# Performance work log

Measured on AMD Instinct MI355X. Metric: run time of the kernel, lower is better.

The kernel has to match this reference:

```python
import jax, jax.numpy as jnp
import numpy as np
from functools import partial

T0, T1, N = 0.0, 1.0, 1024
B = 131072
R, SIGMA = 0.1, 0.2


def setup_inputs() -> dict:
    key = jax.random.key(0)
    k0, k1 = jax.random.split(key)
    Z0 = jax.random.uniform(k0, (B,), dtype=jnp.float32) + 49.5  # around Z0=50 in source
    W = jax.random.normal(k1, (B, N + 1), dtype=jnp.float32)     # Brownian increments (W[:,0] unused)
    Wf = jnp.full((1, 1), R, dtype=jnp.float32)                  # drift weight (f = Linear 1x1)
    Wg = jnp.full((1, 1), SIGMA, dtype=jnp.float32)              # diffusion weight (g = Linear 1x1)
    return {"Z0": Z0, "W": W, "Wf": Wf, "Wg": Wg}


def reference(Z0, W, Wf, Wg):
    # Z[i+1] = Z[i] + f(Z[i])*dt + g(Z[i])*sqrt(dt)*W[i+1], f(z)=Wf*z, g(z)=Wg*z
    dt = jnp.float32((T1 - T0) / N)
    sdt = jnp.sqrt(dt)
    r = Wf[0, 0]
    s = Wg[0, 0]

    def step(z, w):  # z: [B], w: [B]
        zn = z + r * z * dt + s * z * sdt * w
        return zn, zn

    # scan over the N time steps; noise transposed to [N, B]
    _, Zs = jax.lax.scan(step, Z0, jnp.swapaxes(W[:, 1:], 0, 1))
    Z = jnp.concatenate([Z0[:, None], jnp.swapaxes(Zs, 0, 1)], axis=1)  # [B, N+1]
    return Z, W
```

## Files before the change

kernel.cpp:

```cpp
#include <hip/hip_runtime.h>


__global__ __launch_bounds__(256) void em_prefix_kernel(
    const float* __restrict__ Z0,
    const float* __restrict__ W,
    const float* __restrict__ Wf,
    const float* __restrict__ Wg,
    float* __restrict__ Zout,
    float* __restrict__ Wout)
{
    constexpr int NP1  = 1025;
    constexpr int SEG  = 256;
    constexpr int NSEG = 4;

    const int b    = blockIdx.x;
    const int t    = threadIdx.x;
    const int lane = t & 63;
    const int wid  = t >> 6;

    const float dt  = 1.0f / 1024.0f;
    const float sdt = 0.03125f;
    const float a   = Wf[0] * dt;
    const float c   = Wg[0] * sdt;
    const float m0  = 1.0f + a;

    const size_t base = (size_t)b * (size_t)NP1;
    const float* __restrict__ wrow  = W    + base;
    float*       __restrict__ zrow  = Zout + base;
    float*       __restrict__ worow = Wout + base;

    float w[NSEG], m[NSEG];
    #pragma unroll
    for (int s = 0; s < NSEG; ++s) {
        w[s] = wrow[1 + s * SEG + t];
        m[s] = fmaf(c, w[s], m0);
    }

    __shared__ float wtot[NSEG][4];
    float p[NSEG];
    #pragma unroll
    for (int s = 0; s < NSEG; ++s) {
        float v = m[s];
        #pragma unroll
        for (int d = 1; d < 64; d <<= 1) {
            float o = __shfl_up(v, d, 64);
            if (lane >= d) v *= o;
        }
        p[s] = v;
        if (lane == 63) wtot[s][wid] = v;
    }
    __syncthreads();

    const float z0 = Z0[b];
    if (t == 0) {
        zrow[0]  = z0;
        worow[0] = wrow[0];
    }

    float C = z0;
    #pragma unroll
    for (int s = 0; s < NSEG; ++s) {
        float wpre = 1.0f;
        #pragma unroll
        for (int wv = 0; wv < 3; ++wv) {
            float tv = wtot[s][wv];
            if (wv < wid) wpre *= tv;
        }
        const int idx = 1 + s * SEG + t;
        zrow[idx]  = C * wpre * p[s];
        worow[idx] = w[s];
        C *= wtot[s][0] * wtot[s][1] * wtot[s][2] * wtot[s][3];
    }
}

extern "C" void kernel_launch(void* const* d_in, const int* in_sizes, int n_in,
                              void* d_out, int out_size, void* d_ws, size_t ws_size,
                              hipStream_t stream) {
    const float* Z0 = (const float*)d_in[0];
    const float* W  = (const float*)d_in[1];
    const float* Wf = (const float*)d_in[2];
    const float* Wg = (const float*)d_in[3];

    const int B   = in_sizes[0];
    const int NP1 = in_sizes[1] / B;

    float* Zout = (float*)d_out;
    float* Wout = Zout + (size_t)B * (size_t)NP1;

    em_prefix_kernel<<<B, 256, 0, stream>>>(Z0, W, Wf, Wg, Zout, Wout);
}
```

Measured before the change: 301.3 us.

## Use persistent blocks over multiple rows with prefetch and nontemporal memory ops

Switches from one block per row to 4096 blocks, each processing a contiguous range of rows. The loads for the next row's noise are issued before the current row's scan, so memory latency overlaps with compute. Double-buffered shared totals avoid a second barrier per row. All global loads and stores become nontemporal to reduce cache pollution in this streaming kernel. This trades parallelism and occupancy-based latency hiding for fewer block launches and explicit prefetch.

```diff
diff --git a/kernel.cpp b/kernel.cpp
--- a/kernel.cpp
+++ b/kernel.cpp
@@ -7,13 +7,13 @@
     const float* __restrict__ Wf,
     const float* __restrict__ Wg,
     float* __restrict__ Zout,
-    float* __restrict__ Wout)
+    float* __restrict__ Wout,
+    int B, int rowsPerBlock)
 {
     constexpr int NP1  = 1025;
     constexpr int SEG  = 256;
     constexpr int NSEG = 4;
 
-    const int b    = blockIdx.x;
     const int t    = threadIdx.x;
     const int lane = t & 63;
     const int wid  = t >> 6;
@@ -24,52 +24,73 @@
     const float c   = Wg[0] * sdt;
     const float m0  = 1.0f + a;
 
-    const size_t base = (size_t)b * (size_t)NP1;
-    const float* __restrict__ wrow  = W    + base;
-    float*       __restrict__ zrow  = Zout + base;
-    float*       __restrict__ worow = Wout + base;
+    __shared__ float wtot[2][NSEG][4];
 
-    float w[NSEG], m[NSEG];
-    #pragma unroll
-    for (int s = 0; s < NSEG; ++s) {
-        w[s] = wrow[1 + s * SEG + t];
-        m[s] = fmaf(c, w[s], m0);
+    const int r0 = blockIdx.x * rowsPerBlock;
+    const int r1 = min(r0 + rowsPerBlock, B);
+    if (r0 >= r1) return;
+
+    float wcur[NSEG];
+    {
+        const float* __restrict__ wrow = W + (size_t)r0 * NP1;
+        #pragma unroll
+        for (int s = 0; s < NSEG; ++s)
+            wcur[s] = __builtin_nontemporal_load(wrow + 1 + s * SEG + t);
     }
 
-    __shared__ float wtot[NSEG][4];
-    float p[NSEG];
-    #pragma unroll
-    for (int s = 0; s < NSEG; ++s) {
-        float v = m[s];
+    int parity = 0;
+    for (int r = r0; r < r1; ++r) {
+        float wnxt[NSEG];
+        const bool havenext = (r + 1 < r1);
+        if (havenext) {
+            const float* __restrict__ wrown = W + (size_t)(r + 1) * NP1;
+            #pragma unroll
+            for (int s = 0; s < NSEG; ++s)
+                wnxt[s] = __builtin_nontemporal_load(wrown + 1 + s * SEG + t);
+        }
+
+        float p[NSEG];
         #pragma unroll
-        for (int d = 1; d < 64; d <<= 1) {
-            float o = __shfl_up(v, d, 64);
-            if (lane >= d) v *= o;
+        for (int s = 0; s < NSEG; ++s) {
+            float v = fmaf(c, wcur[s], m0);
+            #pragma unroll
+            for (int d = 1; d < 64; d <<= 1) {
+                float o = __shfl_up(v, d, 64);
+                if (lane >= d) v *= o;
+            }
+            p[s] = v;
+            if (lane == 63) wtot[parity][s][wid] = v;
         }
-        p[s] = v;
-        if (lane == 63) wtot[s][wid] = v;
-    }
-    __syncthreads();
+        __syncthreads();
 
-    const float z0 = Z0[b];
-    if (t == 0) {
-        zrow[0]  = z0;
-        worow[0] = wrow[0];
-    }
+        const float  z0   = Z0[r];
+        const size_t base = (size_t)r * NP1;
+        if (t == 0) {
+            __builtin_nontemporal_store(z0, Zout + base);
+            __builtin_nontemporal_store(W[base], Wout + base);
+        }
 
-    float C = z0;
-    #pragma unroll
-    for (int s = 0; s < NSEG; ++s) {
-        float wpre = 1.0f;
+        float C = z0;
         #pragma unroll
-        for (int wv = 0; wv < 3; ++wv) {
-            float tv = wtot[s][wv];
-            if (wv < wid) wpre *= tv;
+        for (int s = 0; s < NSEG; ++s) {
+            float wpre = 1.0f;
+            #pragma unroll
+            for (int wv = 0; wv < 3; ++wv) {
+                float tv = wtot[parity][s][wv];
+                if (wv < wid) wpre *= tv;
+            }
+            const int idx = 1 + s * SEG + t;
+            __builtin_nontemporal_store(C * wpre * p[s], Zout + base + idx);
+            __builtin_nontemporal_store(wcur[s],        Wout + base + idx);
+            C *= wtot[parity][s][0] * wtot[parity][s][1]
+               * wtot[parity][s][2] * wtot[parity][s][3];
         }
-        const int idx = 1 + s * SEG + t;
-        zrow[idx]  = C * wpre * p[s];
-        worow[idx] = w[s];
-        C *= wtot[s][0] * wtot[s][1] * wtot[s][2] * wtot[s][3];
+
+        if (havenext) {
+            #pragma unroll
+            for (int s = 0; s < NSEG; ++s) wcur[s] = wnxt[s];
+        }
+        parity ^= 1;
     }
 }
 
@@ -83,9 +104,12 @@
 
     const int B   = in_sizes[0];
     const int NP1 = in_sizes[1] / B;
+    (void)NP1;
 
     float* Zout = (float*)d_out;
     float* Wout = Zout + (size_t)B * (size_t)NP1;
 
-    em_prefix_kernel<<<B, 256, 0, stream>>>(Z0, W, Wf, Wg, Zout, Wout);
+    const int blocks = 4096;
+    const int rpb    = (B + blocks - 1) / blocks;
+    em_prefix_kernel<<<blocks, 256, 0, stream>>>(Z0, W, Wf, Wg, Zout, Wout, B, rpb);
 }
```

Measured after the change: 495.2 us. 1.64x slower.

## Assign one wavefront per row and drop cross-wave LDS scan synchronisation

Applied to the files above, without the earlier changes.

Each 64-lane wavefront now owns a full row of 1024 steps and processes it as 16 chunks of 64. Each chunk is scanned with shuffles and chained through a carry broadcast from lane 63. This removes the shared-memory wave totals and the __syncthreads barrier, and packs 4 rows per block, so there are far fewer blocks. The W copy-through is now written right after the loads instead of interleaved with the Z stores. The cost is more registers per thread and a longer serial carry chain per wave, and the row length 1025 is now hardcoded on the host side.

```diff
diff --git a/kernel.cpp b/kernel.cpp
--- a/kernel.cpp
+++ b/kernel.cpp
@@ -1,22 +1,22 @@
 #include <hip/hip_runtime.h>
 
 
-__global__ __launch_bounds__(256) void em_prefix_kernel(
+__global__ __launch_bounds__(256) void em_wave_kernel(
     const float* __restrict__ Z0,
     const float* __restrict__ W,
     const float* __restrict__ Wf,
     const float* __restrict__ Wg,
     float* __restrict__ Zout,
-    float* __restrict__ Wout)
+    float* __restrict__ Wout,
+    int B)
 {
-    constexpr int NP1  = 1025;
-    constexpr int SEG  = 256;
-    constexpr int NSEG = 4;
+    constexpr int NP1 = 1025;
+    constexpr int NCH = 16;
 
-    const int b    = blockIdx.x;
-    const int t    = threadIdx.x;
-    const int lane = t & 63;
-    const int wid  = t >> 6;
+    const int lane = threadIdx.x & 63;
+    const int wid  = threadIdx.x >> 6;
+    const int r    = blockIdx.x * 4 + wid;
+    if (r >= B) return;
 
     const float dt  = 1.0f / 1024.0f;
     const float sdt = 0.03125f;
@@ -24,52 +24,43 @@
     const float c   = Wg[0] * sdt;
     const float m0  = 1.0f + a;
 
-    const size_t base = (size_t)b * (size_t)NP1;
+    const size_t base = (size_t)r * NP1;
     const float* __restrict__ wrow  = W    + base;
     float*       __restrict__ zrow  = Zout + base;
     float*       __restrict__ worow = Wout + base;
 
-    float w[NSEG], m[NSEG];
+    float w[NCH];
     #pragma unroll
-    for (int s = 0; s < NSEG; ++s) {
-        w[s] = wrow[1 + s * SEG + t];
-        m[s] = fmaf(c, w[s], m0);
+    for (int k = 0; k < NCH; ++k)
+        w[k] = wrow[1 + 64 * k + lane];
+
+    #pragma unroll
+    for (int k = 0; k < NCH; ++k)
+        worow[1 + 64 * k + lane] = w[k];
+
+    const float z0 = Z0[r];
+    if (lane == 0) {
+        zrow[0]  = z0;
+        worow[0] = wrow[0];
     }
 
-    __shared__ float wtot[NSEG][4];
-    float p[NSEG];
+    float p[NCH];
     #pragma unroll
-    for (int s = 0; s < NSEG; ++s) {
-        float v = m[s];
+    for (int k = 0; k < NCH; ++k) {
+        float v = fmaf(c, w[k], m0);
         #pragma unroll
         for (int d = 1; d < 64; d <<= 1) {
             float o = __shfl_up(v, d, 64);
             if (lane >= d) v *= o;
         }
-        p[s] = v;
-        if (lane == 63) wtot[s][wid] = v;
-    }
-    __syncthreads();
-
-    const float z0 = Z0[b];
-    if (t == 0) {
-        zrow[0]  = z0;
-        worow[0] = wrow[0];
+        p[k] = v;
     }
 
-    float C = z0;
+    float carry = z0;
     #pragma unroll
-    for (int s = 0; s < NSEG; ++s) {
-        float wpre = 1.0f;
-        #pragma unroll
-        for (int wv = 0; wv < 3; ++wv) {
-            float tv = wtot[s][wv];
-            if (wv < wid) wpre *= tv;
-        }
-        const int idx = 1 + s * SEG + t;
-        zrow[idx]  = C * wpre * p[s];
-        worow[idx] = w[s];
-        C *= wtot[s][0] * wtot[s][1] * wtot[s][2] * wtot[s][3];
+    for (int k = 0; k < NCH; ++k) {
+        zrow[1 + 64 * k + lane] = carry * p[k];
+        carry *= __shfl(p[k], 63, 64);
     }
 }
 
@@ -83,9 +74,12 @@
 
     const int B   = in_sizes[0];
     const int NP1 = in_sizes[1] / B;
+    (void)NP1;
 
     float* Zout = (float*)d_out;
-    float* Wout = Zout + (size_t)B * (size_t)NP1;
+    float* Wout = Zout + (size_t)B * 1025;
 
-    em_prefix_kernel<<<B, 256, 0, stream>>>(Z0, W, Wf, Wg, Zout, Wout);
+    const int rowsPerBlock = 4;
+    const int blocks = (B + rowsPerBlock - 1) / rowsPerBlock;
+    em_wave_kernel<<<blocks, 256, 0, stream>>>(Z0, W, Wf, Wg, Zout, Wout, B);
 }
```

Measured after the change: 325.5 us. +8.1%, slower.
